# Kernel tuning notes

Hardware: AMD Instinct MI355X
Metric: run time of the kernel (lower is better)

The kernel has to match this reference:

```python
import math
import jax, jax.numpy as jnp
import numpy as np

C = 1.0          # Poincare ball curvature
NUM_HEADS = 8
EPS = 1e-15

def _beta(a, b):
    # Beta function via lgamma (python float constant)
    return math.exp(math.lgamma(a) + math.lgamma(b) - math.lgamma(a + b))

def h_linear(x, z, r, c=C):
    """HNN++ Poincare fully-connected layer (hypll HLinear).
    x: [..., in] points in the ball; z: [in, out] tangent weights; r: [out] bias."""
    sc = math.sqrt(c)
    x2 = jnp.sum(x * x, axis=-1, keepdims=True)
    lam = 2.0 / (1.0 - c * x2)                                # conformal factor
    zn = jnp.maximum(jnp.linalg.norm(z, axis=0), EPS)          # [out]
    inner = x @ z                                              # [..., out]
    two_scr = 2.0 * sc * r
    d = (2.0 * zn / sc) * jnp.arcsinh(
        (sc * inner * lam / zn) * jnp.cosh(two_scr) - (lam - 1.0) * jnp.sinh(two_scr)
    )
    w = jnp.sinh(sc * d) / sc
    return w / (1.0 + jnp.sqrt(1.0 + c * jnp.sum(w * w, axis=-1, keepdims=True)))

def pairwise_dist(q, k, c=C):
    """Poincare distance d(q,k) = arccosh(1 + 2c|q-k|^2 / ((1-c|q|^2)(1-c|k|^2))) / sqrt(c).
    q,k: [B,H,S,hd] -> [B,H,S,S]."""
    q2 = jnp.sum(q * q, axis=-1)
    k2 = jnp.sum(k * k, axis=-1)
    qk = jnp.einsum('bhqd,bhkd->bhqk', q, k)
    diff2 = jnp.maximum(q2[..., :, None] + k2[..., None, :] - 2.0 * qk, 0.0)
    denom = (1.0 - c * q2)[..., :, None] * (1.0 - c * k2)[..., None, :]
    arg = 1.0 + 2.0 * c * diff2 / denom
    return jnp.arccosh(jnp.maximum(arg, 1.0 + 1e-7)) / math.sqrt(c)

def midpoint(v, w, c=C):
    """Weighted Mobius gyromidpoint: m = 1/2 (x) (sum w*lam*x / sum w*(lam-1)).
    v: [B,H,Sk,hd], w: [B,H,Sq,Sk] -> [B,H,Sq,hd]."""
    v2 = jnp.sum(v * v, axis=-1)                      # [B,H,Sk]
    lam = 2.0 / (1.0 - c * v2)
    num = jnp.einsum('bhqk,bhkd->bhqd', w * lam[..., None, :], v)
    den = jnp.maximum(jnp.einsum('bhqk,bhk->bhq', w, lam - 1.0), EPS)[..., None]
    g = num / den                                     # gyromidpoint pre-scaling
    sc = math.sqrt(c)
    gn = jnp.maximum(jnp.linalg.norm(g, axis=-1, keepdims=True), EPS)
    t = jnp.tanh(0.5 * jnp.arctanh(jnp.clip(sc * gn, 0.0, 1.0 - 1e-7)))
    return (t / sc) * g / gn

def _forward(query, key, value, Wq, bq, Wk, bk, Wv, bv, scale_tau, scale_gamma):
    B, S, E = query.shape
    H = NUM_HEADS
    hd = E // H
    # hyperbolic q/k/v projections, then split into heads: [B,H,S,hd]
    q = h_linear(query, Wq, bq).reshape(B, S, H, hd).transpose(0, 2, 1, 3)
    k = h_linear(key, Wk, bk).reshape(B, S, H, hd).transpose(0, 2, 1, 3)
    v = h_linear(value, Wv, bv).reshape(B, S, H, hd).transpose(0, 2, 1, 3)
    # similarity = -dist/tau - gamma with tau = exp(-scale_tau)
    sim = -pairwise_dist(q, k) * jnp.exp(scale_tau[0]) - scale_gamma[0]
    causal = jnp.triu(jnp.ones((S, S), dtype=bool), k=1)
    sim = jnp.where(causal, -jnp.inf, sim)
    w = jnp.exp(sim)                                  # 'exp' attention activation
    agg = midpoint(v, w)                              # [B,H,S,hd]
    agg = agg.transpose(0, 2, 1, 3).reshape(B, S, E)
    # HNN++ beta-concatenation of the per-head ball points
    scale = _beta(E / 2.0, 0.5) / _beta(hd / 2.0, 0.5)
    return agg * scale

def setup_inputs() -> dict:
    root = jax.random.key(0)
    ks = jax.random.split(root, 8)
    B, S, E = 1, 2048, 512
    s = 0.02  # keep points well inside the unit ball
    return {
        'query': s * jax.random.normal(ks[0], (B, S, E), jnp.float32),
        'key':   s * jax.random.normal(ks[1], (B, S, E), jnp.float32),
        'value': s * jax.random.normal(ks[2], (B, S, E), jnp.float32),
        'Wq': s * jax.random.normal(ks[3], (E, E), jnp.float32),
        'Wk': s * jax.random.normal(ks[4], (E, E), jnp.float32),
        'Wv': s * jax.random.normal(ks[5], (E, E), jnp.float32),
        'bq': jnp.zeros((E,), jnp.float32),
        'bk': jnp.zeros((E,), jnp.float32),
        'bv': jnp.zeros((E,), jnp.float32),
        'scale_tau': jnp.zeros((1,), jnp.float32),
        'scale_gamma': jnp.zeros((1,), jnp.float32),
    }

def reference(query, key, value, Wq, Wk, Wv, bq, bk, bv, scale_tau, scale_gamma):
    return _forward(query, key, value, Wq, bq, Wk, bk, Wv, bv, scale_tau, scale_gamma)
```

## Files before the change

### kernel.cpp

```cpp
#include <hip/hip_runtime.h>
#include <cmath>

#define H 8
#define SEQ 2048
#define EDIM 512
#define HD 64
#define EPSF 1e-15f

typedef short bf16x8 __attribute__((ext_vector_type(8)));
typedef float f32x4 __attribute__((ext_vector_type(4)));

#define ZN_OFF    16
#define STATS_OFF (ZN_OFF + 24 * EDIM)
#define CQ_OFF    (STATS_OFF + 3 * H * SEQ)
#define IK_OFF    (CQ_OFF + H * SEQ)
#define PX2_OFF   (IK_OFF + H * SEQ)
#define U16_OFF   (PX2_OFF + 12288 + 16)
#define WT_U16    0
#define QKVB_U16  (WT_U16 + 3 * EDIM * EDIM)
#define VT_U16    (QKVB_U16 + 3 * SEQ * EDIM)
#define U16_TOTAL (VT_U16 + H * 80 * SEQ)
#define BIG_OFF   (U16_OFF + U16_TOTAL / 2 + 16)
#define TRI16 2112
#define PART_U16S (H * TRI16 * 1280)
#define ACC_FLOATS  (H * SEQ * 80)

__device__ __forceinline__ float bf2f(unsigned short u){
  union { unsigned int i; float f; } v; v.i = ((unsigned int)u) << 16; return v.f;
}
__device__ __forceinline__ unsigned short f2bf(float f){
  union { float f; unsigned int i; } v; v.f = f;
  unsigned int x = v.i;
  unsigned int r = (x + 0x7fffu + ((x >> 16) & 1u)) >> 16;
  return (unsigned short)r;
}

__device__ __forceinline__ unsigned int cvt_pk_bf16(float a, float b){
  unsigned int r;
  asm("v_cvt_pk_bf16_f32 %0, %1, %2" : "=v"(r) : "v"(a), "v"(b));
  return r;
}
__device__ __forceinline__ float vlog2f(float x){
  float r; asm("v_log_f32 %0, %1" : "=v"(r) : "v"(x)); return r;
}
__device__ __forceinline__ float vexp2f(float x){
  float r; asm("v_exp_f32 %0, %1" : "=v"(r) : "v"(x)); return r;
}
__device__ __forceinline__ float vsqrtf(float x){
  float r; asm("v_sqrt_f32 %0, %1" : "=v"(r) : "v"(x)); return r;
}

__device__ __forceinline__ int detect_f32(const unsigned short* __restrict__ q){
  const int l = threadIdx.x & 63;
  float mx = 0.f;
  #pragma unroll
  for (int j = 0; j < 4; ++j) mx = fmaxf(mx, fabsf(bf2f(q[l * 4 + j])));
  #pragma unroll
  for (int m = 32; m >= 1; m >>= 1) mx = fmaxf(mx, __shfl_xor(mx, m, 64));
  return mx > 1000.f;
}

__device__ __forceinline__ int sbase(int s){
  const int a = s >> 2, b = s & 3;
  return s + 2 * a * (a - 1) + a * b;
}

__global__ __launch_bounds__(256) void wcvt_kernel(
    const void* __restrict__ Wq, const void* __restrict__ Wk, const void* __restrict__ Wv,
    const unsigned short* __restrict__ qprobe,
    unsigned short* __restrict__ WT, float* __restrict__ zn)
{
  const int p = blockIdx.y;
  const int bi = blockIdx.x >> 3, bo = blockIdx.x & 7;
  const void* W = (p == 0) ? Wq : ((p == 1) ? Wk : Wv);
  const int t = threadIdx.x;
  const int isf32 = detect_f32(qprobe);
  __shared__ float tile[64][65];

  #pragma unroll
  for (int j = 0; j < 16; ++j){
    int idx = t + 256 * j;
    int il = idx >> 6, ol = idx & 63;
    float val;
    if (isf32) val = ((const float*)W)[(size_t)(bi * 64 + il) * EDIM + bo * 64 + ol];
    else       val = bf2f(((const unsigned short*)W)[(size_t)(bi * 64 + il) * EDIM + bo * 64 + ol]);
    tile[il][ol] = val;
  }
  __syncthreads();
  if (t < 64){
    float s = 0.f;
    #pragma unroll 8
    for (int i = 0; i < 64; ++i){ float v = tile[i][t]; s += v * v; }
    zn[((size_t)(bi * 3 + p)) * EDIM + bo * 64 + t] = s;
  }
  #pragma unroll
  for (int j = 0; j < 16; ++j){
    int idx = t + 256 * j;
    int ol = idx >> 6, il = idx & 63;
    WT[((size_t)p * EDIM + bo * 64 + ol) * EDIM + bi * 64 + il] = f2bf(tile[il][ol]);
  }
}

__global__ __launch_bounds__(256) void hlin_kernel(
    const void* __restrict__ Xq, const void* __restrict__ Xk, const void* __restrict__ Xv,
    const unsigned short* __restrict__ WT,
    const void* __restrict__ Bq, const void* __restrict__ Bk, const void* __restrict__ Bv,
    const float* __restrict__ znacc, const unsigned short* __restrict__ qprobe,
    unsigned short* __restrict__ qkvb, float* __restrict__ stats,
    float* __restrict__ cqs, float* __restrict__ iks,
    unsigned short* __restrict__ VT)
{
  const int p = blockIdx.y;
  const void* X  = (p == 0) ? Xq : ((p == 1) ? Xk : Xv);
  const void* Bb = (p == 0) ? Bq : ((p == 1) ? Bk : Bv);
  const int rg = blockIdx.x;
  const int r0 = rg * 16;
  const int t  = threadIdx.x;
  const int w = t >> 6, lane = t & 63;
  const int col = lane & 15, quad = lane >> 4;
  const int isf32 = detect_f32(qprobe);

  __shared__ float smem[16 * EDIM];
  __shared__ float sw2[16];
  __shared__ float sx2[16];

  const unsigned short* WTb = WT + ((size_t)p * EDIM + w * 128 + col) * EDIM;
  const float* Xf = (const float*)X + (size_t)(r0 + col) * EDIM;
  const unsigned short* Xh = (const unsigned short*)X + (size_t)(r0 + col) * EDIM;

  f32x4 acc[8];
  #pragma unroll
  for (int nt = 0; nt < 8; ++nt) acc[nt] = (f32x4){0.f, 0.f, 0.f, 0.f};
  float x2part = 0.f;

  bf16x8 caf, naf;
  bf16x8 cbf[8], nbf[8];
  {
    if (isf32){
      float4 xa = *(const float4*)&Xf[quad * 8];
      float4 xb = *(const float4*)&Xf[quad * 8 + 4];
      float xv[8] = {xa.x, xa.y, xa.z, xa.w, xb.x, xb.y, xb.z, xb.w};
      #pragma unroll
      for (int j = 0; j < 8; ++j){ caf[j] = (short)f2bf(xv[j]); x2part += xv[j] * xv[j]; }
    } else {
      caf = *(const bf16x8*)&Xh[quad * 8];
      #pragma unroll
      for (int j = 0; j < 8; ++j){ float xv = bf2f((unsigned short)caf[j]); x2part += xv * xv; }
    }
    #pragma unroll
    for (int nt = 0; nt < 8; ++nt)
      cbf[nt] = *(const bf16x8*)&WTb[(size_t)nt * 16 * EDIM + quad * 8];
  }

  for (int ks = 0; ks < 16; ++ks){
    if (ks + 1 < 16){
      const int off = (ks + 1) * 32 + quad * 8;
      if (isf32){
        float4 xa = *(const float4*)&Xf[off];
        float4 xb = *(const float4*)&Xf[off + 4];
        float xv[8] = {xa.x, xa.y, xa.z, xa.w, xb.x, xb.y, xb.z, xb.w};
        #pragma unroll
        for (int j = 0; j < 8; ++j){ naf[j] = (short)f2bf(xv[j]); x2part += xv[j] * xv[j]; }
      } else {
        naf = *(const bf16x8*)&Xh[off];
        #pragma unroll
        for (int j = 0; j < 8; ++j){ float xv = bf2f((unsigned short)naf[j]); x2part += xv * xv; }
      }
      #pragma unroll
      for (int nt = 0; nt < 8; ++nt)
        nbf[nt] = *(const bf16x8*)&WTb[(size_t)nt * 16 * EDIM + off];
    }
    #pragma unroll
    for (int nt = 0; nt < 8; ++nt)
      acc[nt] = __builtin_amdgcn_mfma_f32_16x16x32_bf16(caf, cbf[nt], acc[nt], 0, 0, 0);
    if (ks + 1 < 16){
      caf = naf;
      #pragma unroll
      for (int nt = 0; nt < 8; ++nt) cbf[nt] = nbf[nt];
    }
  }
  x2part += __shfl_xor(x2part, 16, 64);
  x2part += __shfl_xor(x2part, 32, 64);
  if (w == 0 && quad == 0) sx2[col] = x2part;
  __syncthreads();

  float lamr[4], lm1[4];
  #pragma unroll
  for (int r = 0; r < 4; ++r){
    float x2r = sx2[quad * 4 + r];
    lamr[r] = 2.f / (1.f - x2r);
    lm1[r] = lamr[r] - 1.f;
  }
  #pragma unroll
  for (int nt = 0; nt < 8; ++nt){
    const int n = w * 128 + nt * 16 + col;
    float zsum = 0.f;
    #pragma unroll
    for (int bi = 0; bi < 8; ++bi)
      zsum += znacc[((size_t)(bi * 3 + p)) * EDIM + n];
    float znv = fmaxf(sqrtf(zsum), EPSF);
    float rb;
    if (isf32) rb = ((const float*)Bb)[n];
    else       rb = bf2f(((const unsigned short*)Bb)[n]);
    float e2r = __expf(2.f * rb);
    float ie2r = 1.f / e2r;
    float ch = 0.5f * (e2r + ie2r), sh = 0.5f * (e2r - ie2r);
    float izn = 1.f / znv;
    float tz = 2.f * znv;
    #pragma unroll
    for (int r = 0; r < 4; ++r){
      float a = (acc[nt][r] * lamr[r] * izn) * ch - lm1[r] * sh;
      float b = a + sqrtf(a * a + 1.f);
      float tt = __expf(tz * __logf(b));
      smem[(quad * 4 + r) * EDIM + n] = 0.5f * (tt - 1.f / tt);
    }
  }
  __syncthreads();

  {
    int row = t >> 4, l = t & 15;
    float s = 0.f;
    for (int o = l; o < EDIM; o += 16){ float wv = smem[row * EDIM + o]; s += wv * wv; }
    #pragma unroll
    for (int m = 8; m >= 1; m >>= 1) s += __shfl_xor(s, m, 16);
    if (l == 0) sw2[row] = s;
  }
  __syncthreads();

  const int o0 = 2 * t;
  const int h0 = t >> 5;
  const int d0 = o0 & 63;
  const int l5 = t & 31;
  #pragma unroll
  for (int rr = 0; rr < 16; ++rr){
    float inv = 1.f / (1.f + sqrtf(1.f + sw2[rr]));
    unsigned short b0 = f2bf(smem[rr * EDIM + o0] * inv);
    unsigned short b1 = f2bf(smem[rr * EDIM + o0 + 1] * inv);
    float r0v = bf2f(b0), r1v = bf2f(b1);
    int s = r0 + rr;
    unsigned int* dst = (unsigned int*)&qkvb[(((size_t)p * H + h0) * SEQ + s) * HD + d0];
    *dst = (unsigned int)b0 | ((unsigned int)b1 << 16);
    float ss = r0v * r0v + r1v * r1v;
    #pragma unroll
    for (int m = 16; m >= 1; m >>= 1) ss += __shfl_xor(ss, m, 64);
    if (p == 2){
      float lam = 2.f / (1.f - ss);
      VT[((size_t)h0 * 80 + d0) * SEQ + s]     = f2bf(r0v * lam);
      VT[((size_t)h0 * 80 + d0 + 1) * SEQ + s] = f2bf(r1v * lam);
      if (l5 < 16)
        VT[((size_t)h0 * 80 + 64 + l5) * SEQ + s] = (l5 == 0) ? f2bf(lam - 1.f) : 0;
    }
    if (l5 == 0){
      stats[((size_t)p * H + h0) * SEQ + s] = ss;
      if (p == 0) cqs[(size_t)h0 * SEQ + s] = 2.f / (1.f - ss);
      if (p == 1) iks[(size_t)h0 * SEQ + s] = 1.f / (1.f - ss);
    }
  }
}

__device__ __forceinline__ uint4 xpose32(unsigned int tlo0, unsigned int tlo1,
                                         unsigned int thi0, unsigned int thi1,
                                         int srcA, int srcB, int tsel){
  unsigned int a0 = (unsigned int)__shfl((int)tlo0, srcA, 64);
  unsigned int a1 = (unsigned int)__shfl((int)tlo1, srcA, 64);
  unsigned int b0 = (unsigned int)__shfl((int)thi0, srcA, 64);
  unsigned int b1 = (unsigned int)__shfl((int)thi1, srcA, 64);
  unsigned int c0 = (unsigned int)__shfl((int)tlo0, srcB, 64);
  unsigned int c1 = (unsigned int)__shfl((int)tlo1, srcB, 64);
  unsigned int d0 = (unsigned int)__shfl((int)thi0, srcB, 64);
  unsigned int d1 = (unsigned int)__shfl((int)thi1, srcB, 64);
  uint4 r;
  r.x = tsel ? a1 : a0;
  r.y = tsel ? b1 : b0;
  r.z = tsel ? c1 : c0;
  r.w = tsel ? d1 : d0;
  return r;
}

__device__ __forceinline__ void score4(
    const f32x4& s4, const float4& k2v, const float4& ikv,
    float cq, float cqq2, float m2cq, int kbase, int qmax, int quad,
    float m_et, float m_g2, unsigned int& lo, unsigned int& hi)
{
  float w[4];
  #pragma unroll
  for (int r = 0; r < 4; ++r){
    float k2 = (r == 0) ? k2v.x : (r == 1) ? k2v.y : (r == 2) ? k2v.z : k2v.w;
    float ik = (r == 0) ? ikv.x : (r == 1) ? ikv.y : (r == 2) ? ikv.z : ikv.w;
    float t1 = __builtin_fmaf(k2, cq, cqq2);
    t1 = __builtin_fmaf(m2cq, s4[r], t1);
    float u = fmaxf(t1 * ik, 1e-7f);
    float z = 1.f + u + vsqrtf(u * (u + 2.f));
    float wv = vexp2f(__builtin_fmaf(vlog2f(z), m_et, m_g2));
    const int key = kbase + quad * 4 + r;
    w[r] = (key > qmax) ? 0.f : wv;
  }
  lo = cvt_pk_bf16(w[0], w[1]);
  hi = cvt_pk_bf16(w[2], w[3]);
}

template<int NITER>
__device__ __forceinline__ void attn_qloop(
    int s0, int c, int kBeg, int col, int quad, int lane,
    const unsigned short* __restrict__ Qh,
    const bf16x8 (&kf0)[4], const bf16x8 (&kf1)[4],
    const float4 (&ck2)[4], const float4 (&cik)[4],
    const bf16x8 (&vf0)[5], const bf16x8 (&vf1)[5],
    const float* __restrict__ q2s, const float* __restrict__ cqs,
    float m_et, float m_g2, int srcA, int srcB, int tsel,
    float* __restrict__ big, int h, int use_part)
{
  bf16x8 qA0 = *(const bf16x8*)&Qh[(size_t)(s0 * 16 + col) * HD + quad * 8];
  bf16x8 qA1 = *(const bf16x8*)&Qh[(size_t)(s0 * 16 + col) * HD + 32 + quad * 8];
  bf16x8 qB0 = *(const bf16x8*)&Qh[(size_t)((s0 + 1) * 16 + col) * HD + quad * 8];
  bf16x8 qB1 = *(const bf16x8*)&Qh[(size_t)((s0 + 1) * 16 + col) * HD + 32 + quad * 8];
  float q2A = q2s[s0 * 16 + col],       cqA = cqs[s0 * 16 + col];
  float q2B = q2s[(s0 + 1) * 16 + col], cqB = cqs[(s0 + 1) * 16 + col];

  #pragma unroll
  for (int i = 0; i < NITER; ++i){
    const int sA = s0 + 2 * i, sB = sA + 1;
    bf16x8 nA0, nA1, nB0, nB1;
    float nq2A, ncqA, nq2B, ncqB;
    if (i + 1 < NITER){
      const int tA = (sA + 2) * 16 + col, tB = (sA + 3) * 16 + col;
      nA0 = *(const bf16x8*)&Qh[(size_t)tA * HD + quad * 8];
      nA1 = *(const bf16x8*)&Qh[(size_t)tA * HD + 32 + quad * 8];
      nB0 = *(const bf16x8*)&Qh[(size_t)tB * HD + quad * 8];
      nB1 = *(const bf16x8*)&Qh[(size_t)tB * HD + 32 + quad * 8];
      nq2A = q2s[tA]; ncqA = cqs[tA];
      nq2B = q2s[tB]; ncqB = cqs[tB];
    }

    const float cqq2A = cqA * q2A, m2cqA = -2.f * cqA;
    const float cqq2B = cqB * q2B, m2cqB = -2.f * cqB;
    const int qmaxA = sA * 16 + col, qmaxB = sB * 16 + col;

    f32x4 sSA[4], sSB[4];
    __builtin_amdgcn_s_setprio(1);
    #pragma unroll
    for (int g = 0; g < 4; ++g){
      f32x4 z4 = (f32x4){0.f, 0.f, 0.f, 0.f};
      sSA[g] = __builtin_amdgcn_mfma_f32_16x16x32_bf16(kf0[g], qA0, z4, 0, 0, 0);
      sSA[g] = __builtin_amdgcn_mfma_f32_16x16x32_bf16(kf1[g], qA1, sSA[g], 0, 0, 0);
      sSB[g] = __builtin_amdgcn_mfma_f32_16x16x32_bf16(kf0[g], qB0, z4, 0, 0, 0);
      sSB[g] = __builtin_amdgcn_mfma_f32_16x16x32_bf16(kf1[g], qB1, sSB[g], 0, 0, 0);
    }
    __builtin_amdgcn_s_setprio(0);

    unsigned int loA[4], hiA[4], loB[4], hiB[4];
    #pragma unroll
    for (int g = 0; g < 4; ++g){
      score4(sSA[g], ck2[g], cik[g], cqA, cqq2A, m2cqA, kBeg + g * 16, qmaxA, quad,
             m_et, m_g2, loA[g], hiA[g]);
      score4(sSB[g], ck2[g], cik[g], cqB, cqq2B, m2cqB, kBeg + g * 16, qmaxB, quad,
             m_et, m_g2, loB[g], hiB[g]);
    }

    union { uint4 u; bf16x8 v; } pA01, pA23, pB01, pB23;
    pA01.u = xpose32(loA[0], loA[1], hiA[0], hiA[1], srcA, srcB, tsel);
    pA23.u = xpose32(loA[2], loA[3], hiA[2], hiA[3], srcA, srcB, tsel);
    pB01.u = xpose32(loB[0], loB[1], hiB[0], hiB[1], srcA, srcB, tsel);
    pB23.u = xpose32(loB[2], loB[3], hiB[2], hiB[3], srcA, srcB, tsel);

    f32x4 pvA[5], pvB[5];
    __builtin_amdgcn_s_setprio(1);
    #pragma unroll
    for (int nt = 0; nt < 5; ++nt){
      f32x4 z4 = (f32x4){0.f, 0.f, 0.f, 0.f};
      pvA[nt] = __builtin_amdgcn_mfma_f32_16x16x32_bf16(pA01.v, vf0[nt], z4, 0, 0, 0);
      pvA[nt] = __builtin_amdgcn_mfma_f32_16x16x32_bf16(pA23.v, vf1[nt], pvA[nt], 0, 0, 0);
      pvB[nt] = __builtin_amdgcn_mfma_f32_16x16x32_bf16(pB01.v, vf0[nt], z4, 0, 0, 0);
      pvB[nt] = __builtin_amdgcn_mfma_f32_16x16x32_bf16(pB23.v, vf1[nt], pvB[nt], 0, 0, 0);
    }
    __builtin_amdgcn_s_setprio(0);

    if (use_part){
      uint2* slotA = (uint2*)big + (size_t)(h * TRI16 + sbase(sA) + c) * 320;
      uint2* slotB = (uint2*)big + (size_t)(h * TRI16 + sbase(sB) + c) * 320;
      #pragma unroll
      for (int nt = 0; nt < 5; ++nt){
        uint2 pk;
        pk.x = cvt_pk_bf16(pvA[nt][0], pvA[nt][1]);
        pk.y = cvt_pk_bf16(pvA[nt][2], pvA[nt][3]);
        slotA[nt * 64 + lane] = pk;
        pk.x = cvt_pk_bf16(pvB[nt][0], pvB[nt][1]);
        pk.y = cvt_pk_bf16(pvB[nt][2], pvB[nt][3]);
        slotB[nt * 64 + lane] = pk;
      }
    } else {
      #pragma unroll
      for (int r = 0; r < 4; ++r){
        float* rowA = big + ((size_t)h * SEQ + sA * 16 + quad * 4 + r) * 80;
        float* rowB = big + ((size_t)h * SEQ + sB * 16 + quad * 4 + r) * 80;
        #pragma unroll
        for (int nt = 0; nt < 5; ++nt){
          atomicAdd(&rowA[16 * nt + col], pvA[nt][r]);
          atomicAdd(&rowB[16 * nt + col], pvB[nt][r]);
        }
      }
    }

    if (i + 1 < NITER){
      qA0 = nA0; qA1 = nA1; qB0 = nB0; qB1 = nB1;
      q2A = nq2A; cqA = ncqA; q2B = nq2B; cqB = ncqB;
    }
  }
}

__global__ __launch_bounds__(64, 2) void attn_kernel(
    const unsigned short* __restrict__ Qb, const unsigned short* __restrict__ Kb,
    const unsigned short* __restrict__ VT,
    const float* __restrict__ q2s_all, const float* __restrict__ k2s_all,
    const float* __restrict__ cqs_all, const float* __restrict__ iks_all,
    const void* __restrict__ tau, const void* __restrict__ gam,
    const unsigned short* __restrict__ qprobe,
    float* __restrict__ big, int use_part)
{
  const int h = blockIdx.y;
  const int c = blockIdx.x >> 4;
  const int j = blockIdx.x & 15;
  const int nsl = (33 - c) >> 1;
  if (j >= nsl) return;
  const int kBeg = c * 64;
  const int s0 = 4 * c + 8 * j;
  const int rem = 128 - s0;
  const int lane = threadIdx.x;
  const int col = lane & 15, quad = lane >> 4;

  const unsigned short* Qh  = Qb + (size_t)h * SEQ * HD;
  const unsigned short* Kh  = Kb + (size_t)h * SEQ * HD;
  const unsigned short* VTh = VT + (size_t)h * 80 * SEQ;
  const float* q2s = q2s_all + (size_t)h * SEQ;
  const float* k2s = k2s_all + (size_t)h * SEQ;
  const float* cqs = cqs_all + (size_t)h * SEQ;
  const float* iks = iks_all + (size_t)h * SEQ;

  const int isf32 = detect_f32(qprobe);
  float tauv, gamv;
  if (isf32){ tauv = ((const float*)tau)[0]; gamv = ((const float*)gam)[0]; }
  else      { tauv = bf2f(((const unsigned short*)tau)[0]);
              gamv = bf2f(((const unsigned short*)gam)[0]); }
  const float m_et = -__expf(tauv);
  const float m_g2 = -gamv * 1.44269504088896340736f;

  const int srcA = ((quad & 1) * 2) * 16 + col;
  const int srcB = srcA + 16;
  const int tsel = quad >> 1;

  bf16x8 kf0[4], kf1[4];
  float4 ck2[4], cik[4];
  #pragma unroll
  for (int g = 0; g < 4; ++g){
    kf0[g] = *(const bf16x8*)&Kh[(size_t)(kBeg + g * 16 + col) * HD + quad * 8];
    kf1[g] = *(const bf16x8*)&Kh[(size_t)(kBeg + g * 16 + col) * HD + 32 + quad * 8];
    ck2[g] = *(const float4*)&k2s[kBeg + g * 16 + quad * 4];
    cik[g] = *(const float4*)&iks[kBeg + g * 16 + quad * 4];
  }
  bf16x8 vf0[5], vf1[5];
  #pragma unroll
  for (int nt = 0; nt < 5; ++nt){
    vf0[nt] = *(const bf16x8*)&VTh[(size_t)(16 * nt + col) * SEQ + kBeg + quad * 8];
    vf1[nt] = *(const bf16x8*)&VTh[(size_t)(16 * nt + col) * SEQ + kBeg + 32 + quad * 8];
  }

  if (rem >= 8)
    attn_qloop<4>(s0, c, kBeg, col, quad, lane, Qh, kf0, kf1, ck2, cik, vf0, vf1,
                  q2s, cqs, m_et, m_g2, srcA, srcB, tsel, big, h, use_part);
  else
    attn_qloop<2>(s0, c, kBeg, col, quad, lane, Qh, kf0, kf1, ck2, cik, vf0, vf1,
                  q2s, cqs, m_et, m_g2, srcA, srcB, tsel, big, h, use_part);
}

__global__ __launch_bounds__(256) void attn_fin_kernel(
    const float* __restrict__ big, int use_part,
    float* __restrict__ out, float beta_scale)
{
  const int h = blockIdx.y, s = blockIdx.x;
  const int t = threadIdx.x;
  const int w = t >> 6, lane = t & 63;
  const int col = lane & 15, quad = lane >> 4;
  const int q0 = s * 16;

  __shared__ float red[4][64][20];

  f32x4 pv[5];
  #pragma unroll
  for (int nt = 0; nt < 5; ++nt) pv[nt] = (f32x4){0.f, 0.f, 0.f, 0.f};

  if (use_part){
    const int tbase = sbase(s);
    const int nv = (s >> 2) + 1;
    for (int sl = w; sl < nv; sl += 4){
      const uint2* slot = (const uint2*)big + (size_t)(h * TRI16 + tbase + sl) * 320;
      #pragma unroll
      for (int nt = 0; nt < 5; ++nt){
        uint2 v = slot[nt * 64 + lane];
        pv[nt][0] += bf2f((unsigned short)(v.x & 0xffffu));
        pv[nt][1] += bf2f((unsigned short)(v.x >> 16));
        pv[nt][2] += bf2f((unsigned short)(v.y & 0xffffu));
        pv[nt][3] += bf2f((unsigned short)(v.y >> 16));
      }
    }
  } else if (w == 0){
    #pragma unroll
    for (int nt = 0; nt < 5; ++nt)
      #pragma unroll
      for (int r = 0; r < 4; ++r)
        pv[nt][r] = big[((size_t)h * SEQ + q0 + quad * 4 + r) * 80 + 16 * nt + col];
  }

  #pragma unroll
  for (int nt = 0; nt < 5; ++nt)
    *(float4*)&red[w][lane][nt * 4] = (float4){pv[nt][0], pv[nt][1], pv[nt][2], pv[nt][3]};
  __syncthreads();

  if (t < 64){
    #pragma unroll
    for (int nt = 0; nt < 5; ++nt){
      float4 a = *(const float4*)&red[0][t][nt * 4];
      float4 b = *(const float4*)&red[1][t][nt * 4];
      float4 c = *(const float4*)&red[2][t][nt * 4];
      float4 d = *(const float4*)&red[3][t][nt * 4];
      pv[nt][0] = a.x + b.x + c.x + d.x;
      pv[nt][1] = a.y + b.y + c.y + d.y;
      pv[nt][2] = a.z + b.z + c.z + d.z;
      pv[nt][3] = a.w + b.w + c.w + d.w;
    }
    #pragma unroll
    for (int r = 0; r < 4; ++r){
      float den = __shfl(pv[4][r], quad * 16, 64);
      den = fmaxf(den, EPSF);
      float inv_den = 1.f / den;
      float g[4];
      float gsq = 0.f;
      #pragma unroll
      for (int nt = 0; nt < 4; ++nt){ g[nt] = pv[nt][r] * inv_den; gsq += g[nt] * g[nt]; }
      #pragma unroll
      for (int m = 8; m >= 1; m >>= 1) gsq += __shfl_xor(gsq, m, 64);
      float gn = fmaxf(sqrtf(gsq), EPSF);
      float x = fminf(gn, 1.f - 1e-7f);
      float tt2 = x / (1.f + sqrtf(1.f - x * x));
      float scl = (tt2 / gn) * beta_scale;
      const int q = q0 + quad * 4 + r;
      #pragma unroll
      for (int nt = 0; nt < 4; ++nt)
        out[(size_t)q * EDIM + h * HD + 16 * nt + col] = g[nt] * scl;
    }
  }
}

extern "C" void kernel_launch(void* const* d_in, const int* in_sizes, int n_in,
                              void* d_out, int out_size, void* d_ws, size_t ws_size,
                              hipStream_t stream){
  const void* Xq  = d_in[0];
  const void* Xk  = d_in[1];
  const void* Xv  = d_in[2];
  const void* Wq  = d_in[3];
  const void* Wk  = d_in[4];
  const void* Wv  = d_in[5];
  const void* Bq  = d_in[6];
  const void* Bk  = d_in[7];
  const void* Bv  = d_in[8];
  const void* tau = d_in[9];
  const void* gam = d_in[10];

  float* wsf   = (float*)d_ws;
  float* zn    = wsf + ZN_OFF;
  float* stats = wsf + STATS_OFF;
  float* cqs   = wsf + CQ_OFF;
  float* iks   = wsf + IK_OFF;
  unsigned short* u16b = (unsigned short*)(wsf + U16_OFF);
  unsigned short* WT   = u16b + WT_U16;
  unsigned short* qkvb = u16b + QKVB_U16;
  unsigned short* VT   = u16b + VT_U16;
  float* big   = wsf + BIG_OFF;

  const int use_part =
      (ws_size >= (size_t)BIG_OFF * sizeof(float) + (size_t)PART_U16S * 2) ? 1 : 0;

  unsigned short* Qb = qkvb;
  unsigned short* Kb = qkvb + (size_t)H * SEQ * HD;
  float* q2s = stats;
  float* k2s = stats + (size_t)H * SEQ;
  const unsigned short* qprobe = (const unsigned short*)Xq;

  double lb1 = lgamma(EDIM / 2.0) + lgamma(0.5) - lgamma(EDIM / 2.0 + 0.5);
  double lb2 = lgamma(HD / 2.0)   + lgamma(0.5) - lgamma(HD / 2.0 + 0.5);
  float beta_scale = (float)exp(lb1 - lb2);

  wcvt_kernel<<<dim3(64, 3), dim3(256), 0, stream>>>(Wq, Wk, Wv, qprobe, WT, zn);
  hlin_kernel<<<dim3(128, 3), dim3(256), 0, stream>>>(
      Xq, Xk, Xv, WT, Bq, Bk, Bv, zn, qprobe, qkvb, stats, cqs, iks, VT);
  if (!use_part)
    hipMemsetAsync(big, 0, (size_t)ACC_FLOATS * sizeof(float), stream);
  attn_kernel<<<dim3(512, H), dim3(64), 0, stream>>>(
      Qb, Kb, VT, q2s, k2s, cqs, iks, tau, gam, qprobe, big, use_part);
  attn_fin_kernel<<<dim3(128, H), dim3(256), 0, stream>>>(
      big, use_part, (float*)d_out, beta_scale);
}
```

Measured before the change: 188.0 us.

## Split hlin GEMM K dimension across two wave groups with LDS reduction

Doubles the hlin_kernel block to 512 threads, with each pair of waves splitting the 512-long reduction dimension into two halves. Partial accumulators are exchanged and summed through shared memory, and each wave then finishes the epilogue for half of its column tiles. The epilogue row loops are also spread across the extra threads. This is meant to shorten the serial MFMA chain per wave and raise occupancy in the projection kernel, at the cost of an extra LDS round trip and barrier.

New measurement: 242.6 us. 29.1% more time.

```diff
diff --git a/kernel.cpp b/kernel.cpp
--- a/kernel.cpp
+++ b/kernel.cpp
@@ -101,7 +101,7 @@
   }
 }
 
-__global__ __launch_bounds__(256) void hlin_kernel(
+__global__ __launch_bounds__(512) void hlin_kernel(
     const void* __restrict__ Xq, const void* __restrict__ Xk, const void* __restrict__ Xv,
     const unsigned short* __restrict__ WT,
     const void* __restrict__ Bq, const void* __restrict__ Bk, const void* __restrict__ Bv,
@@ -116,17 +116,19 @@
   const int rg = blockIdx.x;
   const int r0 = rg * 16;
   const int t  = threadIdx.x;
-  const int w = t >> 6, lane = t & 63;
+  const int w8 = t >> 6, lane = t & 63;
+  const int cg = w8 >> 1, ks = w8 & 1;
   const int col = lane & 15, quad = lane >> 4;
   const int isf32 = detect_f32(qprobe);
 
   __shared__ float smem[16 * EDIM];
   __shared__ float sw2[16];
-  __shared__ float sx2[16];
-
-  const unsigned short* WTb = WT + ((size_t)p * EDIM + w * 128 + col) * EDIM;
-  const float* Xf = (const float*)X + (size_t)(r0 + col) * EDIM;
-  const unsigned short* Xh = (const unsigned short*)X + (size_t)(r0 + col) * EDIM;
+  __shared__ float sx2[2][16];
+
+  const int koff = ks * 256;
+  const unsigned short* WTb = WT + ((size_t)p * EDIM + cg * 128 + col) * EDIM + koff;
+  const float* Xf = (const float*)X + (size_t)(r0 + col) * EDIM + koff;
+  const unsigned short* Xh = (const unsigned short*)X + (size_t)(r0 + col) * EDIM + koff;
 
   f32x4 acc[8];
   #pragma unroll
@@ -152,9 +154,9 @@
       cbf[nt] = *(const bf16x8*)&WTb[(size_t)nt * 16 * EDIM + quad * 8];
   }
 
-  for (int ks = 0; ks < 16; ++ks){
-    if (ks + 1 < 16){
-      const int off = (ks + 1) * 32 + quad * 8;
+  for (int st = 0; st < 8; ++st){
+    if (st + 1 < 8){
+      const int off = (st + 1) * 32 + quad * 8;
       if (isf32){
         float4 xa = *(const float4*)&Xf[off];
         float4 xb = *(const float4*)&Xf[off + 4];
@@ -173,7 +175,7 @@
     #pragma unroll
     for (int nt = 0; nt < 8; ++nt)
       acc[nt] = __builtin_amdgcn_mfma_f32_16x16x32_bf16(caf, cbf[nt], acc[nt], 0, 0, 0);
-    if (ks + 1 < 16){
+    if (st + 1 < 8){
       caf = naf;
       #pragma unroll
       for (int nt = 0; nt < 8; ++nt) cbf[nt] = nbf[nt];
@@ -181,19 +183,41 @@
   }
   x2part += __shfl_xor(x2part, 16, 64);
   x2part += __shfl_xor(x2part, 32, 64);
-  if (w == 0 && quad == 0) sx2[col] = x2part;
+  if (cg == 0 && quad == 0) sx2[ks][col] = x2part;
+
+  {
+    const int park = (ks == 0) ? 4 : 0;
+    #pragma unroll
+    for (int j = 0; j < 4; ++j){
+      const int nt = park + j;
+      const int n = cg * 128 + nt * 16 + col;
+      #pragma unroll
+      for (int r = 0; r < 4; ++r)
+        smem[(quad * 4 + r) * EDIM + n] = acc[nt][r];
+    }
+  }
   __syncthreads();
+  const int ntb = ks * 4;
+  #pragma unroll
+  for (int j = 0; j < 4; ++j){
+    const int nt = ntb + j;
+    const int n = cg * 128 + nt * 16 + col;
+    #pragma unroll
+    for (int r = 0; r < 4; ++r)
+      acc[nt][r] += smem[(quad * 4 + r) * EDIM + n];
+  }
 
   float lamr[4], lm1[4];
   #pragma unroll
   for (int r = 0; r < 4; ++r){
-    float x2r = sx2[quad * 4 + r];
+    float x2r = sx2[0][quad * 4 + r] + sx2[1][quad * 4 + r];
     lamr[r] = 2.f / (1.f - x2r);
     lm1[r] = lamr[r] - 1.f;
   }
   #pragma unroll
-  for (int nt = 0; nt < 8; ++nt){
-    const int n = w * 128 + nt * 16 + col;
+  for (int j = 0; j < 4; ++j){
+    const int nt = ntb + j;
+    const int n = cg * 128 + nt * 16 + col;
     float zsum = 0.f;
     #pragma unroll
     for (int bi = 0; bi < 8; ++bi)
@@ -218,21 +242,24 @@
   __syncthreads();
 
   {
-    int row = t >> 4, l = t & 15;
+    int row = t >> 5, l = t & 31;
     float s = 0.f;
-    for (int o = l; o < EDIM; o += 16){ float wv = smem[row * EDIM + o]; s += wv * wv; }
-    #pragma unroll
-    for (int m = 8; m >= 1; m >>= 1) s += __shfl_xor(s, m, 16);
+    for (int o = l; o < EDIM; o += 32){ float wv = smem[row * EDIM + o]; s += wv * wv; }
+    #pragma unroll
+    for (int m = 16; m >= 1; m >>= 1) s += __shfl_xor(s, m, 32);
     if (l == 0) sw2[row] = s;
   }
   __syncthreads();
 
-  const int o0 = 2 * t;
-  const int h0 = t >> 5;
+  const int th = t & 255;
+  const int half = t >> 8;
+  const int o0 = 2 * th;
+  const int h0 = th >> 5;
   const int d0 = o0 & 63;
-  const int l5 = t & 31;
-  #pragma unroll
-  for (int rr = 0; rr < 16; ++rr){
+  const int l5 = th & 31;
+  #pragma unroll
+  for (int jr = 0; jr < 8; ++jr){
+    const int rr = half * 8 + jr;
     float inv = 1.f / (1.f + sqrtf(1.f + sw2[rr]));
     unsigned short b0 = f2bf(smem[rr * EDIM + o0] * inv);
     unsigned short b1 = f2bf(smem[rr * EDIM + o0 + 1] * inv);
@@ -590,7 +617,7 @@
   float beta_scale = (float)exp(lb1 - lb2);
 
   wcvt_kernel<<<dim3(64, 3), dim3(256), 0, stream>>>(Wq, Wk, Wv, qprobe, WT, zn);
-  hlin_kernel<<<dim3(128, 3), dim3(256), 0, stream>>>(
+  hlin_kernel<<<dim3(128, 3), dim3(512), 0, stream>>>(
       Xq, Xk, Xv, WT, Bq, Bk, Bv, zn, qprobe, qkvb, stats, cqs, iks, VT);
   if (!use_part)
     hipMemsetAsync(big, 0, (size_t)ACC_FLOATS * sizeof(float), stream);
```

## Split HLinear into column-halved GEMM kernel plus separate finalize kernel

Applied to the files above, without the earlier changes.

The fused HLinear kernel is split in two. A GEMM kernel now handles half the output columns per block, doubling the grid to 768 blocks, writes the unnormalized sinh outputs as bf16 to a scratch buffer, and stores per-row partial squared norms. A second kernel sums the partials, applies the ball normalization and writes Q/K/V, stats and VT. This raises parallelism and drops the 32KB shared tile, at the cost of an extra launch, an intermediate global round trip, and an extra bf16 rounding before normalization.

Measured after the change: 192.1 us. 1.02x slower.

```diff
diff --git a/kernel.cpp b/kernel.cpp
--- a/kernel.cpp
+++ b/kernel.cpp
@@ -101,40 +101,39 @@
   }
 }
 
-__global__ __launch_bounds__(256) void hlin_kernel(
+__global__ __launch_bounds__(256) void hlin_gemm_kernel(
     const void* __restrict__ Xq, const void* __restrict__ Xk, const void* __restrict__ Xv,
     const unsigned short* __restrict__ WT,
     const void* __restrict__ Bq, const void* __restrict__ Bk, const void* __restrict__ Bv,
     const float* __restrict__ znacc, const unsigned short* __restrict__ qprobe,
-    unsigned short* __restrict__ qkvb, float* __restrict__ stats,
-    float* __restrict__ cqs, float* __restrict__ iks,
-    unsigned short* __restrict__ VT)
+    unsigned short* __restrict__ wtmp, float* __restrict__ prow)
 {
   const int p = blockIdx.y;
   const void* X  = (p == 0) ? Xq : ((p == 1) ? Xk : Xv);
   const void* Bb = (p == 0) ? Bq : ((p == 1) ? Bk : Bv);
-  const int rg = blockIdx.x;
+  const int rg = blockIdx.x >> 1;
+  const int ch = blockIdx.x & 1;
   const int r0 = rg * 16;
+  const int c0 = ch * 256;
   const int t  = threadIdx.x;
-  const int w = t >> 6, lane = t & 63;
+  const int w4 = t >> 6, lane = t & 63;
   const int col = lane & 15, quad = lane >> 4;
   const int isf32 = detect_f32(qprobe);
 
-  __shared__ float smem[16 * EDIM];
-  __shared__ float sw2[16];
   __shared__ float sx2[16];
-
-  const unsigned short* WTb = WT + ((size_t)p * EDIM + w * 128 + col) * EDIM;
+  __shared__ float partq[4][16];
+
+  const unsigned short* WTb = WT + ((size_t)p * EDIM + c0 + w4 * 64 + col) * EDIM;
   const float* Xf = (const float*)X + (size_t)(r0 + col) * EDIM;
   const unsigned short* Xh = (const unsigned short*)X + (size_t)(r0 + col) * EDIM;
 
-  f32x4 acc[8];
-  #pragma unroll
-  for (int nt = 0; nt < 8; ++nt) acc[nt] = (f32x4){0.f, 0.f, 0.f, 0.f};
+  f32x4 acc[4];
+  #pragma unroll
+  for (int nt = 0; nt < 4; ++nt) acc[nt] = (f32x4){0.f, 0.f, 0.f, 0.f};
   float x2part = 0.f;
 
   bf16x8 caf, naf;
-  bf16x8 cbf[8], nbf[8];
+  bf16x8 cbf[4], nbf[4];
   {
     if (isf32){
       float4 xa = *(const float4*)&Xf[quad * 8];
@@ -148,13 +147,13 @@
       for (int j = 0; j < 8; ++j){ float xv = bf2f((unsigned short)caf[j]); x2part += xv * xv; }
     }
     #pragma unroll
-    for (int nt = 0; nt < 8; ++nt)
+    for (int nt = 0; nt < 4; ++nt)
       cbf[nt] = *(const bf16x8*)&WTb[(size_t)nt * 16 * EDIM + quad * 8];
   }
 
-  for (int ks = 0; ks < 16; ++ks){
-    if (ks + 1 < 16){
-      const int off = (ks + 1) * 32 + quad * 8;
+  for (int st = 0; st < 16; ++st){
+    if (st + 1 < 16){
+      const int off = (st + 1) * 32 + quad * 8;
       if (isf32){
         float4 xa = *(const float4*)&Xf[off];
         float4 xb = *(const float4*)&Xf[off + 4];
@@ -167,21 +166,21 @@
         for (int j = 0; j < 8; ++j){ float xv = bf2f((unsigned short)naf[j]); x2part += xv * xv; }
       }
       #pragma unroll
-      for (int nt = 0; nt < 8; ++nt)
+      for (int nt = 0; nt < 4; ++nt)
         nbf[nt] = *(const bf16x8*)&WTb[(size_t)nt * 16 * EDIM + off];
     }
     #pragma unroll
-    for (int nt = 0; nt < 8; ++nt)
+    for (int nt = 0; nt < 4; ++nt)
       acc[nt] = __builtin_amdgcn_mfma_f32_16x16x32_bf16(caf, cbf[nt], acc[nt], 0, 0, 0);
-    if (ks + 1 < 16){
+    if (st + 1 < 16){
       caf = naf;
       #pragma unroll
-      for (int nt = 0; nt < 8; ++nt) cbf[nt] = nbf[nt];
+      for (int nt = 0; nt < 4; ++nt) cbf[nt] = nbf[nt];
     }
   }
   x2part += __shfl_xor(x2part, 16, 64);
   x2part += __shfl_xor(x2part, 32, 64);
-  if (w == 0 && quad == 0) sx2[col] = x2part;
+  if (w4 == 0 && quad == 0) sx2[col] = x2part;
   __syncthreads();
 
   float lamr[4], lm1[4];
@@ -191,9 +190,11 @@
     lamr[r] = 2.f / (1.f - x2r);
     lm1[r] = lamr[r] - 1.f;
   }
-  #pragma unroll
-  for (int nt = 0; nt < 8; ++nt){
-    const int n = w * 128 + nt * 16 + col;
+
+  float rsql[4] = {0.f, 0.f, 0.f, 0.f};
+  #pragma unroll
+  for (int nt = 0; nt < 4; ++nt){
+    const int n = c0 + w4 * 64 + nt * 16 + col;
     float zsum = 0.f;
     #pragma unroll
     for (int bi = 0; bi < 8; ++bi)
@@ -204,26 +205,50 @@
     else       rb = bf2f(((const unsigned short*)Bb)[n]);
     float e2r = __expf(2.f * rb);
     float ie2r = 1.f / e2r;
-    float ch = 0.5f * (e2r + ie2r), sh = 0.5f * (e2r - ie2r);
+    float chv = 0.5f * (e2r + ie2r), sh = 0.5f * (e2r - ie2r);
     float izn = 1.f / znv;
     float tz = 2.f * znv;
     #pragma unroll
     for (int r = 0; r < 4; ++r){
-      float a = (acc[nt][r] * lamr[r] * izn) * ch - lm1[r] * sh;
+      float a = (acc[nt][r] * lamr[r] * izn) * chv - lm1[r] * sh;
       float b = a + sqrtf(a * a + 1.f);
       float tt = __expf(tz * __logf(b));
-      smem[(quad * 4 + r) * EDIM + n] = 0.5f * (tt - 1.f / tt);
-    }
+      float wv = 0.5f * (tt - 1.f / tt);
+      rsql[r] += wv * wv;
+      wtmp[((size_t)p * SEQ + r0 + quad * 4 + r) * EDIM + n] = f2bf(wv);
+    }
+  }
+  #pragma unroll
+  for (int r = 0; r < 4; ++r){
+    #pragma unroll
+    for (int m = 8; m >= 1; m >>= 1) rsql[r] += __shfl_xor(rsql[r], m, 16);
+  }
+  if (col == 0){
+    #pragma unroll
+    for (int r = 0; r < 4; ++r) partq[w4][quad * 4 + r] = rsql[r];
   }
   __syncthreads();
-
-  {
-    int row = t >> 4, l = t & 15;
-    float s = 0.f;
-    for (int o = l; o < EDIM; o += 16){ float wv = smem[row * EDIM + o]; s += wv * wv; }
-    #pragma unroll
-    for (int m = 8; m >= 1; m >>= 1) s += __shfl_xor(s, m, 16);
-    if (l == 0) sw2[row] = s;
+  if (t < 16){
+    float s = partq[0][t] + partq[1][t] + partq[2][t] + partq[3][t];
+    prow[(((size_t)p * 128 + rg) * 2 + ch) * 16 + t] = s;
+  }
+}
+
+__global__ __launch_bounds__(256) void hlin_fin_kernel(
+    const unsigned short* __restrict__ wtmp, const float* __restrict__ prow,
+    unsigned short* __restrict__ qkvb, float* __restrict__ stats,
+    float* __restrict__ cqs, float* __restrict__ iks,
+    unsigned short* __restrict__ VT)
+{
+  const int p = blockIdx.y;
+  const int rg = blockIdx.x;
+  const int r0 = rg * 16;
+  const int t  = threadIdx.x;
+
+  __shared__ float sw2[16];
+  if (t < 16){
+    sw2[t] = prow[(((size_t)p * 128 + rg) * 2 + 0) * 16 + t] +
+             prow[(((size_t)p * 128 + rg) * 2 + 1) * 16 + t];
   }
   __syncthreads();
 
@@ -234,10 +259,13 @@
   #pragma unroll
   for (int rr = 0; rr < 16; ++rr){
     float inv = 1.f / (1.f + sqrtf(1.f + sw2[rr]));
-    unsigned short b0 = f2bf(smem[rr * EDIM + o0] * inv);
-    unsigned short b1 = f2bf(smem[rr * EDIM + o0 + 1] * inv);
+    const int s = r0 + rr;
+    unsigned int wu = *(const unsigned int*)&wtmp[((size_t)p * SEQ + s) * EDIM + o0];
+    float w0 = bf2f((unsigned short)(wu & 0xffffu));
+    float w1 = bf2f((unsigned short)(wu >> 16));
+    unsigned short b0 = f2bf(w0 * inv);
+    unsigned short b1 = f2bf(w1 * inv);
     float r0v = bf2f(b0), r1v = bf2f(b1);
-    int s = r0 + rr;
     unsigned int* dst = (unsigned int*)&qkvb[(((size_t)p * H + h0) * SEQ + s) * HD + d0];
     *dst = (unsigned int)b0 | ((unsigned int)b1 << 16);
     float ss = r0v * r0v + r1v * r1v;
@@ -570,11 +598,13 @@
   float* stats = wsf + STATS_OFF;
   float* cqs   = wsf + CQ_OFF;
   float* iks   = wsf + IK_OFF;
+  float* prow  = wsf + PX2_OFF;
   unsigned short* u16b = (unsigned short*)(wsf + U16_OFF);
   unsigned short* WT   = u16b + WT_U16;
   unsigned short* qkvb = u16b + QKVB_U16;
   unsigned short* VT   = u16b + VT_U16;
   float* big   = wsf + BIG_OFF;
+  unsigned short* wtmp = (unsigned short*)big;
 
   const int use_part =
       (ws_size >= (size_t)BIG_OFF * sizeof(float) + (size_t)PART_U16S * 2) ? 1 : 0;
@@ -590,8 +620,10 @@
   float beta_scale = (float)exp(lb1 - lb2);
 
   wcvt_kernel<<<dim3(64, 3), dim3(256), 0, stream>>>(Wq, Wk, Wv, qprobe, WT, zn);
-  hlin_kernel<<<dim3(128, 3), dim3(256), 0, stream>>>(
-      Xq, Xk, Xv, WT, Bq, Bk, Bv, zn, qprobe, qkvb, stats, cqs, iks, VT);
+  hlin_gemm_kernel<<<dim3(256, 3), dim3(256), 0, stream>>>(
+      Xq, Xk, Xv, WT, Bq, Bk, Bv, zn, qprobe, wtmp, prow);
+  hlin_fin_kernel<<<dim3(128, 3), dim3(256), 0, stream>>>(
+      wtmp, prow, qkvb, stats, cqs, iks, VT);
   if (!use_part)
     hipMemsetAsync(big, 0, (size_t)ACC_FLOATS * sizeof(float), stream);
   attn_kernel<<<dim3(512, H), dim3(64), 0, stream>>>(
```
